# Kernel tuning notes

Measured on AMD Instinct MI355X. Metric: run time of the kernel, lower is better.

Reference implementation:

```python
import jax, jax.numpy as jnp
import numpy as np

N_C = 50000
N_N = 50000
E = 500000
D = 128


def _graph_conv(x_src, src, dst, n_src, n_dst, W, b):
    # DGL GraphConv, norm='both': symmetric degree normalization, then linear.
    ones = jnp.ones(src.shape, x_src.dtype)
    deg_out = jax.ops.segment_sum(ones, src, num_segments=n_src)
    deg_in = jax.ops.segment_sum(ones, dst, num_segments=n_dst)
    norm_src = jnp.maximum(deg_out, 1.0) ** -0.5  # [n_src]
    norm_dst = jnp.maximum(deg_in, 1.0) ** -0.5   # [n_dst]
    m = (x_src * norm_src[:, None])[src]          # [E, D] gather
    agg = jax.ops.segment_sum(m, dst, num_segments=n_dst)  # [n_dst, D]
    return (agg * norm_dst[:, None]) @ W + b


def _sage_conv(x_src, x_dst, src, dst, n_dst, W_self, W_neigh, b):
    # DGL SAGEConv, aggregator='mean': fc_self(h_dst) + fc_neigh(mean_neigh) + bias.
    ones = jnp.ones(src.shape, x_src.dtype)
    deg_in = jnp.maximum(jax.ops.segment_sum(ones, dst, num_segments=n_dst), 1.0)
    h_neigh = jax.ops.segment_sum(x_src[src], dst, num_segments=n_dst) / deg_in[:, None]
    return x_dst @ W_self + h_neigh @ W_neigh + b


def setup_inputs() -> dict:
    key = jax.random.key(0)
    ks = jax.random.split(key, 20)
    s = 1.0 / np.sqrt(D)
    inp = {
        'feat_C': jax.random.normal(ks[0], (N_C, D), jnp.float32),
        'feat_N': jax.random.normal(ks[1], (N_N, D), jnp.float32),
        'W1_cc': jax.random.normal(ks[2], (D, D), jnp.float32) * s,
        'b1_cc': jnp.zeros((D,), jnp.float32),
        'W1_cn': jax.random.normal(ks[3], (D, D), jnp.float32) * s,
        'b1_cn': jnp.zeros((D,), jnp.float32),
        'W1_self': jax.random.normal(ks[4], (D, D), jnp.float32) * s,
        'W1_neigh': jax.random.normal(ks[5], (D, D), jnp.float32) * s,
        'b1_nn': jnp.zeros((D,), jnp.float32),
        'W2_cc': jax.random.normal(ks[6], (D, D), jnp.float32) * s,
        'b2_cc': jnp.zeros((D,), jnp.float32),
        'W2_cn': jax.random.normal(ks[7], (D, D), jnp.float32) * s,
        'b2_cn': jnp.zeros((D,), jnp.float32),
        'W2_self': jax.random.normal(ks[8], (D, D), jnp.float32) * s,
        'W2_neigh': jax.random.normal(ks[9], (D, D), jnp.float32) * s,
        'b2_nn': jnp.zeros((D,), jnp.float32),
        'cc_src': jax.random.randint(ks[10], (E,), 0, N_C),
        'cc_dst': jax.random.randint(ks[11], (E,), 0, N_C),
        'cn_src': jax.random.randint(ks[12], (E,), 0, N_C),
        'cn_dst': jax.random.randint(ks[13], (E,), 0, N_N),
        'nn_src': jax.random.randint(ks[14], (E,), 0, N_N),
        'nn_dst': jax.random.randint(ks[15], (E,), 0, N_N),
    }
    return inp


def reference(feat_C, feat_N, W1_cc, b1_cc, W1_cn, b1_cn, W1_self, W1_neigh, b1_nn,
              W2_cc, b2_cc, W2_cn, b2_cn, W2_self, W2_neigh, b2_nn,
              cc_src, cc_dst, cn_src, cn_dst, nn_src, nn_dst):
    # layer 1 (HeteroGraphConv, aggregate='sum') + relu
    hC = _graph_conv(feat_C, cc_src, cc_dst, N_C, N_C, W1_cc, b1_cc)
    hN = (_graph_conv(feat_C, cn_src, cn_dst, N_C, N_N, W1_cn, b1_cn)
          + _sage_conv(feat_N, feat_N, nn_src, nn_dst, N_N, W1_self, W1_neigh, b1_nn))
    hC = jax.nn.relu(hC)
    hN = jax.nn.relu(hN)
    # layer 2
    oC = _graph_conv(hC, cc_src, cc_dst, N_C, N_C, W2_cc, b2_cc)
    oN = (_graph_conv(hC, cn_src, cn_dst, N_C, N_N, W2_cn, b2_cn)
          + _sage_conv(hN, hN, nn_src, nn_dst, N_N, W2_self, W2_neigh, b2_nn))
    return oC, oN
```

## Files before the change

kernel.cpp:

```cpp
#include <hip/hip_runtime.h>

#define NCN 50000
#define NE  500000
#define DF  128

#define BSHIFT 9
#define NBUCK 98
#define BK 128
#define CAP 7168
#define CHUNK 4096

typedef __attribute__((ext_vector_type(8))) short mfrag;
typedef __attribute__((ext_vector_type(4))) float facc4;

__device__ inline ushort f2bf(float x) {
    unsigned u = __float_as_uint(x);
    unsigned r = (u + 0x7FFFu + ((u >> 16) & 1u)) >> 16;
    return (ushort)r;
}
__device__ inline float bf2f(ushort h) { return __uint_as_float(((unsigned)h) << 16); }

__device__ inline void store_split(ushort* __restrict__ T, int row, int lane,
                                   float vx, float vy) {
    ushort hx = f2bf(vx); ushort lx = f2bf(vx - bf2f(hx));
    ushort hy = f2bf(vy); ushort ly = f2bf(vy - bf2f(hy));
    uint hp = (uint)hx | ((uint)hy << 16);
    uint lp = (uint)lx | ((uint)ly << 16);
    *(uint*)(T + (size_t)row * DF + lane * 2) = hp;
    *(uint*)(T + (size_t)NCN * DF + (size_t)row * DF + lane * 2) = lp;
}

__global__ __launch_bounds__(256) void hist2_k(
    const int* __restrict__ cc_src, const int* __restrict__ cn_src,
    int* __restrict__ cnt2)
{
    int i = blockIdx.x * 256 + threadIdx.x;
    if (i >= NE) return;
    atomicAdd(&cnt2[cc_src[i]], 1);
    atomicAdd(&cnt2[NCN + cn_src[i]], 1);
}

__global__ __launch_bounds__(256) void srcnorm_k(
    const int* __restrict__ cnt2, float* __restrict__ snorm2, int n2)
{
    int i = blockIdx.x * 256 + threadIdx.x;
    if (i >= n2) return;
    int c = cnt2[i]; if (c < 1) c = 1;
    snorm2[i] = rsqrtf((float)c);
}

__global__ __launch_bounds__(256) void binA_k(
    const int* __restrict__ cc_src, const int* __restrict__ cc_dst,
    const int* __restrict__ cn_src, const int* __restrict__ cn_dst,
    const int* __restrict__ nn_src, const int* __restrict__ nn_dst,
    uint2* __restrict__ R, int* __restrict__ bc)
{
    const int s = blockIdx.y;
    const int* key; const int* pay;
    switch (s) {
      case 0: key = cc_dst; pay = cc_src; break;
      case 1: key = cn_dst; pay = cn_src; break;
      default: key = nn_dst; pay = nn_src; break;
    }
    __shared__ uint2 rec[CHUNK];
    __shared__ int lhist[BK], lofs[BK], lcur[BK], gbase[BK];
    __shared__ int ls[256];
    const int tid = threadIdx.x;
    const int base = blockIdx.x * CHUNK;

    int k[16], p[16];
    #pragma unroll
    for (int j = 0; j < 16; ++j) {
        int e = base + j * 256 + tid;
        bool valid = (e < NE);
        k[j] = valid ? key[e] : -1;
        p[j] = valid ? pay[e] : 0;
    }
    if (tid < BK) lhist[tid] = 0;
    __syncthreads();
    #pragma unroll
    for (int j = 0; j < 16; ++j)
        if (k[j] >= 0) atomicAdd(&lhist[k[j] >> BSHIFT], 1);
    __syncthreads();
    int v = (tid < BK) ? lhist[tid] : 0;
    ls[tid] = v;
    __syncthreads();
    #pragma unroll
    for (int off = 1; off < 128; off <<= 1) {
        int t = (tid >= off) ? ls[tid - off] : 0;
        __syncthreads();
        ls[tid] += t;
        __syncthreads();
    }
    if (tid < BK) { int e = ls[tid] - v; lofs[tid] = e; lcur[tid] = e; }
    __syncthreads();
    #pragma unroll
    for (int j = 0; j < 16; ++j) {
        if (k[j] >= 0) {
            int b = k[j] >> BSHIFT;
            int pos = atomicAdd(&lcur[b], 1);
            rec[pos] = make_uint2((unsigned)k[j], (unsigned)p[j]);
        }
    }
    __syncthreads();
    if (tid < BK) {
        int c = lcur[tid] - lofs[tid];
        gbase[tid] = (c > 0) ? atomicAdd(&bc[s * BK + tid], c) : 0;
    }
    __syncthreads();
    int total = ls[127];
    for (int i = tid; i < total; i += 256) {
        uint2 r = rec[i];
        int b = (int)(r.x >> BSHIFT);
        int gi = gbase[b] + (i - lofs[b]);
        R[((size_t)s * NBUCK + b) * CAP + gi] = r;
    }
}

__global__ __launch_bounds__(256) void binB_k(
    const uint2* __restrict__ R, const int* __restrict__ bc,
    int* __restrict__ rp3, int* __restrict__ col3)
{
    const int b = blockIdx.x;
    const int s = blockIdx.y;
    const int tid = threadIdx.x;
    __shared__ int cnt[512];
    __shared__ int lofs[512];
    __shared__ int ls[256];
    __shared__ int sbase;

    const int nrec = bc[s * BK + b];
    const uint2* rec = R + ((size_t)s * NBUCK + b) * CAP;

    for (int i = tid; i < 512; i += 256) cnt[i] = 0;
    __syncthreads();
    for (int i = tid; i < nrec; i += 256)
        atomicAdd(&cnt[rec[i].x & 511], 1);
    __syncthreads();

    {
        int v = (tid < b) ? bc[s * BK + tid] : 0;
        ls[tid] = v;
        __syncthreads();
        for (int off = 128; off > 0; off >>= 1) {
            if (tid < off) ls[tid] += ls[tid + off];
            __syncthreads();
        }
        if (tid == 0) sbase = ls[0];
        __syncthreads();
    }
    const int colBase = sbase;

    int v0 = cnt[2 * tid], v1 = cnt[2 * tid + 1];
    int pairSum = v0 + v1;
    ls[tid] = pairSum;
    __syncthreads();
    #pragma unroll
    for (int off = 1; off < 256; off <<= 1) {
        int t = (tid >= off) ? ls[tid - off] : 0;
        __syncthreads();
        ls[tid] += t;
        __syncthreads();
    }
    int excl = ls[tid] - pairSum;
    lofs[2 * tid] = excl;
    lofs[2 * tid + 1] = excl + v0;
    __syncthreads();
    const int total = ls[255];

    int* rp = rp3 + (size_t)s * (NCN + 1);
    for (int j = tid; j < 512; j += 256) {
        int d = b * 512 + j;
        if (d < NCN) rp[d] = colBase + lofs[j];
    }
    if (b == NBUCK - 1 && tid == 0) rp[NCN] = colBase + total;
    __syncthreads();

    int* col = col3 + (size_t)s * NE + colBase;
    for (int i = tid; i < nrec; i += 256) {
        uint2 r = rec[i];
        int pos = atomicAdd(&lofs[r.x & 511], 1);
        col[pos] = (int)r.y;
    }
}

__global__ __launch_bounds__(256) void wconv_k(
    const float* __restrict__ Wm0, const float* __restrict__ Wm1,
    const float* __restrict__ Wm2, const float* __restrict__ Wm3,
    const float* __restrict__ Wm4, const float* __restrict__ Wm5,
    const float* __restrict__ Wm6, const float* __restrict__ Wm7,
    ushort* __restrict__ out)
{
    const float* Ws[8] = {Wm0, Wm1, Wm2, Wm3, Wm4, Wm5, Wm6, Wm7};
    const float* W = Ws[blockIdx.x];
    ushort* o = out + (size_t)blockIdx.x * 32768;
    for (int i = threadIdx.x; i < 16384; i += 256) {
        int c = i >> 13;
        int r = i & 8191;
        int n = r >> 6;
        int jj = r & 63;
        int kk = c * 64 + (jj ^ ((n & 7) << 3));
        float wv = W[kk * 128 + n];
        ushort h = f2bf(wv);
        float lv = wv - bf2f(h);
        o[c * 16384 + r] = h;
        o[c * 16384 + 8192 + r] = f2bf(lv);
    }
}

__global__ __launch_bounds__(256) void agg_k(
    const float* __restrict__ X0, const int* __restrict__ rp0,
    const int* __restrict__ col0, const float* __restrict__ sc0,
    ushort* __restrict__ out0,
    const float* __restrict__ X1, const int* __restrict__ rp1,
    const int* __restrict__ col1, const float* __restrict__ sc1,
    ushort* __restrict__ out1,
    const float* __restrict__ X2, const int* __restrict__ rp2,
    const int* __restrict__ col2, const float* __restrict__ sc2,
    ushort* __restrict__ out2)
{
    const float* X; const int* rp; const int* col; const float* sc; ushort* out;
    if (blockIdx.y == 0)      { X = X0; rp = rp0; col = col0; sc = sc0; out = out0; }
    else if (blockIdx.y == 1) { X = X1; rp = rp1; col = col1; sc = sc1; out = out1; }
    else                      { X = X2; rp = rp2; col = col2; sc = sc2; out = out2; }

    int gid = blockIdx.x * 256 + threadIdx.x;
    int row = gid >> 6;
    int lane = threadIdx.x & 63;
    if (row >= NCN) return;
    int e0 = rp[row], e1 = rp[row + 1];
    float ax = 0.f, ay = 0.f;
    int e = e0;
    for (; e + 4 <= e1; e += 4) {
        int s0 = col[e], s1 = col[e + 1], s2 = col[e + 2], s3 = col[e + 3];
        float c0 = sc ? sc[s0] : 1.0f;
        float c1 = sc ? sc[s1] : 1.0f;
        float c2 = sc ? sc[s2] : 1.0f;
        float c3 = sc ? sc[s3] : 1.0f;
        const float2 u0 = *(const float2*)(X + (size_t)s0 * DF + lane * 2);
        const float2 u1 = *(const float2*)(X + (size_t)s1 * DF + lane * 2);
        const float2 u2 = *(const float2*)(X + (size_t)s2 * DF + lane * 2);
        const float2 u3 = *(const float2*)(X + (size_t)s3 * DF + lane * 2);
        ax = fmaf(u0.x, c0, ax); ay = fmaf(u0.y, c0, ay);
        ax = fmaf(u1.x, c1, ax); ay = fmaf(u1.y, c1, ay);
        ax = fmaf(u2.x, c2, ax); ay = fmaf(u2.y, c2, ay);
        ax = fmaf(u3.x, c3, ax); ay = fmaf(u3.y, c3, ay);
    }
    for (; e < e1; ++e) {
        int s0 = col[e];
        float c0 = sc ? sc[s0] : 1.0f;
        const float2 u0 = *(const float2*)(X + (size_t)s0 * DF + lane * 2);
        ax = fmaf(u0.x, c0, ax); ay = fmaf(u0.y, c0, ay);
    }
    int deg = e1 - e0; if (deg < 1) deg = 1;
    float dsc = sc ? rsqrtf((float)deg) : (1.0f / (float)deg);
    store_split(out, row, lane, ax * dsc, ay * dsc);
}

template<int NSRC, bool RELU, int F32S>
__global__ __launch_bounds__(256, 4) void mgemm_k(
    const void* __restrict__ A0, const void* __restrict__ A1, const void* __restrict__ A2,
    const ushort* __restrict__ Wi0, const ushort* __restrict__ Wi1, const ushort* __restrict__ Wi2,
    const float* __restrict__ b0, const float* __restrict__ b1,
    float* __restrict__ Y, int M)
{
    constexpr int NCH = 2 * NSRC;
    __shared__ ushort Wsm[16384];
    const int tid = threadIdx.x;
    const int l = tid & 63;
    const int wv = tid >> 6;
    const int r0 = blockIdx.x * 128;

    const void*   Aarr[3] = {A0, A1, A2};
    const ushort* Warr[3] = {Wi0, Wi1, Wi2};

    int arow[2];
    #pragma unroll
    for (int rt = 0; rt < 2; ++rt) {
        int r = r0 + wv * 32 + rt * 16 + (l & 15);
        arow[rt] = (r < M) ? r : (M - 1);
    }
    const int kgrp = (l >> 4) * 8;

    facc4 acc[2][8];
    #pragma unroll
    for (int rt = 0; rt < 2; ++rt)
        #pragma unroll
        for (int ct = 0; ct < 8; ++ct)
            acc[rt][ct] = (facc4){0.f, 0.f, 0.f, 0.f};

    uint4 Wr[8];
    auto loadWr = [&](int c) {
        int s = c >> 1, half = c & 1;
        const uint4* wp = (const uint4*)(Warr[s] + half * 16384);
        #pragma unroll
        for (int i = 0; i < 8; ++i) Wr[i] = wp[i * 256 + tid];
    };

    mfrag ah[2][2], al[2][2];
    auto loadA = [&](int c) {
        int s = c >> 1;
        int k0 = (c & 1) * 64;
        if (s == F32S) {
            const float* F = (const float*)Aarr[s];
            #pragma unroll
            for (int ks = 0; ks < 2; ++ks)
                #pragma unroll
                for (int rt = 0; rt < 2; ++rt) {
                    const float* p = F + (size_t)arow[rt] * DF + k0 + ks * 32 + kgrp;
                    float4 v0 = *(const float4*)p;
                    float4 v1 = *(const float4*)(p + 4);
                    union { mfrag m; ushort u[8]; } H, L;
                    float vv0[4] = {v0.x, v0.y, v0.z, v0.w};
                    float vv1[4] = {v1.x, v1.y, v1.z, v1.w};
                    #pragma unroll
                    for (int j = 0; j < 4; ++j) {
                        ushort h = f2bf(vv0[j]);
                        H.u[j] = h; L.u[j] = f2bf(vv0[j] - bf2f(h));
                    }
                    #pragma unroll
                    for (int j = 0; j < 4; ++j) {
                        ushort h = f2bf(vv1[j]);
                        H.u[4 + j] = h; L.u[4 + j] = f2bf(vv1[j] - bf2f(h));
                    }
                    ah[ks][rt] = H.m; al[ks][rt] = L.m;
                }
        } else {
            const ushort* T = (const ushort*)Aarr[s];
            #pragma unroll
            for (int ks = 0; ks < 2; ++ks)
                #pragma unroll
                for (int rt = 0; rt < 2; ++rt) {
                    size_t o = (size_t)arow[rt] * DF + k0 + ks * 32 + kgrp;
                    ah[ks][rt] = *(const mfrag*)(T + o);
                    al[ks][rt] = *(const mfrag*)(T + (size_t)NCN * DF + o);
                }
        }
    };

    loadWr(0);
    #pragma unroll
    for (int c = 0; c < NCH; ++c) {
        __syncthreads();
        {
            uint4* wd = (uint4*)Wsm;
            #pragma unroll
            for (int i = 0; i < 8; ++i) wd[i * 256 + tid] = Wr[i];
        }
        loadA(c);
        if (c + 1 < NCH) loadWr(c + 1);
        __syncthreads();
        #pragma unroll
        for (int ks = 0; ks < 2; ++ks) {
            const int kbyte = ks * 64 + (l >> 4) * 16;
            #pragma unroll
            for (int ct = 0; ct < 8; ++ct) {
                int colc = ct * 16 + (l & 15);
                int widx = colc * 64 + ((kbyte ^ ((colc & 7) << 4)) >> 1);
                mfrag w_hi = *(const mfrag*)(Wsm + widx);
                mfrag w_lo = *(const mfrag*)(Wsm + 8192 + widx);
                #pragma unroll
                for (int rt = 0; rt < 2; ++rt) {
                    acc[rt][ct] = __builtin_amdgcn_mfma_f32_16x16x32_bf16(ah[ks][rt], w_hi, acc[rt][ct], 0, 0, 0);
                    acc[rt][ct] = __builtin_amdgcn_mfma_f32_16x16x32_bf16(ah[ks][rt], w_lo, acc[rt][ct], 0, 0, 0);
                    acc[rt][ct] = __builtin_amdgcn_mfma_f32_16x16x32_bf16(al[ks][rt], w_hi, acc[rt][ct], 0, 0, 0);
                }
            }
        }
    }
    __syncthreads();

    float bias[8];
    #pragma unroll
    for (int ct = 0; ct < 8; ++ct) {
        int colc = ct * 16 + (l & 15);
        float bv = b0 ? b0[colc] : 0.f;
        if (b1) bv += b1[colc];
        bias[ct] = bv;
    }
    #pragma unroll
    for (int rt = 0; rt < 2; ++rt) {
        #pragma unroll
        for (int q = 0; q < 4; ++q) {
            int row = r0 + wv * 32 + rt * 16 + (l >> 4) * 4 + q;
            if (row < M) {
                #pragma unroll
                for (int ct = 0; ct < 8; ++ct) {
                    float v = acc[rt][ct][q] + bias[ct];
                    if (RELU) v = fmaxf(v, 0.f);
                    Y[(size_t)row * DF + ct * 16 + (l & 15)] = v;
                }
            }
        }
    }
}

extern "C" void kernel_launch(void* const* d_in, const int* in_sizes, int n_in,
                              void* d_out, int out_size, void* d_ws, size_t ws_size,
                              hipStream_t stream)
{
    (void)in_sizes; (void)n_in; (void)out_size; (void)ws_size;
    const float* feat_C   = (const float*)d_in[0];
    const float* feat_N   = (const float*)d_in[1];
    const float* W1_cc    = (const float*)d_in[2];
    const float* b1_cc    = (const float*)d_in[3];
    const float* W1_cn    = (const float*)d_in[4];
    const float* b1_cn    = (const float*)d_in[5];
    const float* W1_self  = (const float*)d_in[6];
    const float* W1_neigh = (const float*)d_in[7];
    const float* b1_nn    = (const float*)d_in[8];
    const float* W2_cc    = (const float*)d_in[9];
    const float* b2_cc    = (const float*)d_in[10];
    const float* W2_cn    = (const float*)d_in[11];
    const float* b2_cn    = (const float*)d_in[12];
    const float* W2_self  = (const float*)d_in[13];
    const float* W2_neigh = (const float*)d_in[14];
    const float* b2_nn    = (const float*)d_in[15];
    const int* cc_src = (const int*)d_in[16];
    const int* cc_dst = (const int*)d_in[17];
    const int* cn_src = (const int*)d_in[18];
    const int* cn_dst = (const int*)d_in[19];
    const int* nn_src = (const int*)d_in[20];
    const int* nn_dst = (const int*)d_in[21];

    char* ws = (char*)d_ws;
    size_t off = 0;
    auto take = [&](size_t bytes) -> char* {
        char* p = ws + off;
        off = (off + bytes + 255) & ~(size_t)255;
        return p;
    };
    int*    rp3    = (int*)take((size_t)3 * (NCN + 1) * sizeof(int));
    int*    col3   = (int*)take((size_t)3 * NE * sizeof(int));
    float*  snorm2 = (float*)take((size_t)2 * NCN * sizeof(float));
    int*    cnt2   = (int*)take((size_t)2 * NCN * sizeof(int));
    int*    bc     = (int*)take((size_t)3 * BK * sizeof(int));
    ushort* Wimg   = (ushort*)take((size_t)8 * 32768 * sizeof(ushort));
    char* bigRegion = take((size_t)2 * 2 * NCN * DF * sizeof(ushort));
    uint2*  R  = (uint2*)bigRegion;
    ushort* P0 = (ushort*)bigRegion;
    ushort* P1 = (ushort*)(bigRegion + (size_t)2 * NCN * DF * sizeof(ushort));

    float* oC = (float*)d_out;
    float* oN = oC + (size_t)NCN * DF;
    ushort* oCsplit = (ushort*)oC;

    const int edgeBlocks = (NE + 255) / 256;
    const int binABlocks = (NE + CHUNK - 1) / CHUNK;
    const int aggBlocks  = (NCN * 64 + 255) / 256;
    const int gemmBlocks = (NCN + 127) / 128;

    auto img = [&](int m) { return (const ushort*)(Wimg + (size_t)m * 32768); };
    const int* rpCC = rp3 + 0 * (NCN + 1);
    const int* rpCN = rp3 + 1 * (NCN + 1);
    const int* rpNN = rp3 + 2 * (NCN + 1);
    const int* colCC = col3 + 0 * NE;
    const int* colCN = col3 + 1 * NE;
    const int* colNN = col3 + 2 * NE;
    const float* snCC = snorm2 + 0 * NCN;
    const float* snCN = snorm2 + 1 * NCN;

    hipMemsetAsync(cnt2, 0, (size_t)2 * NCN * sizeof(int), stream);
    hipMemsetAsync(bc, 0, (size_t)3 * BK * sizeof(int), stream);
    hist2_k<<<edgeBlocks, 256, 0, stream>>>(cc_src, cn_src, cnt2);
    srcnorm_k<<<(2 * NCN + 255) / 256, 256, 0, stream>>>(cnt2, snorm2, 2 * NCN);
    binA_k<<<dim3(binABlocks, 3), 256, 0, stream>>>(cc_src, cc_dst, cn_src, cn_dst,
                                                    nn_src, nn_dst, R, bc);
    binB_k<<<dim3(NBUCK, 3), 256, 0, stream>>>(R, bc, rp3, col3);
    wconv_k<<<8, 256, 0, stream>>>(W1_cc, W1_cn, W1_neigh, W1_self,
                                   W2_cc, W2_cn, W2_neigh, W2_self, Wimg);

    agg_k<<<dim3(aggBlocks, 3), 256, 0, stream>>>(
        feat_C, rpCC, colCC, snCC, P0,
        feat_C, rpCN, colCN, snCN, P1,
        feat_N, rpNN, colNN, nullptr, oCsplit);
    mgemm_k<3, true, 2><<<gemmBlocks, 256, 0, stream>>>(P1, oCsplit, feat_N,
                                                        img(1), img(2), img(3),
                                                        b1_cn, b1_nn, oN, NCN);
    mgemm_k<1, true, -1><<<gemmBlocks, 256, 0, stream>>>(P0, nullptr, nullptr,
                                                         img(0), nullptr, nullptr,
                                                         b1_cc, nullptr, oC, NCN);

    agg_k<<<dim3(aggBlocks, 2), 256, 0, stream>>>(
        oC, rpCC, colCC, snCC, P0,
        oC, rpCN, colCN, snCN, P1,
        nullptr, nullptr, nullptr, nullptr, nullptr);
    agg_k<<<dim3(aggBlocks, 1), 256, 0, stream>>>(
        oN, rpNN, colNN, nullptr, oCsplit,
        nullptr, nullptr, nullptr, nullptr, nullptr,
        nullptr, nullptr, nullptr, nullptr, nullptr);
    mgemm_k<3, false, 2><<<gemmBlocks, 256, 0, stream>>>(P1, oCsplit, oN,
                                                         img(5), img(6), img(7),
                                                         b2_cn, b2_nn, oN, NCN);
    mgemm_k<1, false, -1><<<gemmBlocks, 256, 0, stream>>>(P0, nullptr, nullptr,
                                                          img(4), nullptr, nullptr,
                                                          b2_cc, nullptr, oC, NCN);
}
```

Baseline: 485.2 us.

## Aggregate two rows per wave with float4 gathers and double-buffer GEMM A loads

The aggregation kernel now gives each half-wave one destination row and gathers 16-byte float4 chunks per lane. Neighbour indices and scales are loaded cooperatively once per 32-edge chunk and broadcast with shuffles, which cuts redundant index and scale loads and widens memory transactions. The GEMM kernel double-buffers the A fragments so the next chunk's A load overlaps the current MFMA work. Its occupancy hint drops from 4 to 3 blocks to make room for the extra registers, trading occupancy for overlap.

```diff
diff --git a/kernel.cpp b/kernel.cpp
--- a/kernel.cpp
+++ b/kernel.cpp
@@ -20,14 +20,16 @@
 }
 __device__ inline float bf2f(ushort h) { return __uint_as_float(((unsigned)h) << 16); }
 
-__device__ inline void store_split(ushort* __restrict__ T, int row, int lane,
-                                   float vx, float vy) {
-    ushort hx = f2bf(vx); ushort lx = f2bf(vx - bf2f(hx));
-    ushort hy = f2bf(vy); ushort ly = f2bf(vy - bf2f(hy));
-    uint hp = (uint)hx | ((uint)hy << 16);
-    uint lp = (uint)lx | ((uint)ly << 16);
-    *(uint*)(T + (size_t)row * DF + lane * 2) = hp;
-    *(uint*)(T + (size_t)NCN * DF + (size_t)row * DF + lane * 2) = lp;
+__device__ inline void store_split4(ushort* __restrict__ T, int row, int lane4,
+                                    float4 v) {
+    ushort h0 = f2bf(v.x); ushort l0 = f2bf(v.x - bf2f(h0));
+    ushort h1 = f2bf(v.y); ushort l1 = f2bf(v.y - bf2f(h1));
+    ushort h2 = f2bf(v.z); ushort l2 = f2bf(v.z - bf2f(h2));
+    ushort h3 = f2bf(v.w); ushort l3 = f2bf(v.w - bf2f(h3));
+    uint2 hp = make_uint2((uint)h0 | ((uint)h1 << 16), (uint)h2 | ((uint)h3 << 16));
+    uint2 lp = make_uint2((uint)l0 | ((uint)l1 << 16), (uint)l2 | ((uint)l3 << 16));
+    *(uint2*)(T + (size_t)row * DF + lane4 * 4) = hp;
+    *(uint2*)(T + (size_t)NCN * DF + (size_t)row * DF + lane4 * 4) = lp;
 }
 
 __global__ __launch_bounds__(256) void hist2_k(
@@ -224,41 +226,55 @@
     else if (blockIdx.y == 1) { X = X1; rp = rp1; col = col1; sc = sc1; out = out1; }
     else                      { X = X2; rp = rp2; col = col2; sc = sc2; out = out2; }
 
-    int gid = blockIdx.x * 256 + threadIdx.x;
-    int row = gid >> 6;
-    int lane = threadIdx.x & 63;
+    int wid = (blockIdx.x * 256 + threadIdx.x) >> 6;
+    int half = (threadIdx.x >> 5) & 1;
+    int lane4 = threadIdx.x & 31;
+    int row = wid * 2 + half;
     if (row >= NCN) return;
     int e0 = rp[row], e1 = rp[row + 1];
-    float ax = 0.f, ay = 0.f;
+    const bool useSc = (sc != nullptr);
+    float4 a = make_float4(0.f, 0.f, 0.f, 0.f);
     int e = e0;
-    for (; e + 4 <= e1; e += 4) {
-        int s0 = col[e], s1 = col[e + 1], s2 = col[e + 2], s3 = col[e + 3];
-        float c0 = sc ? sc[s0] : 1.0f;
-        float c1 = sc ? sc[s1] : 1.0f;
-        float c2 = sc ? sc[s2] : 1.0f;
-        float c3 = sc ? sc[s3] : 1.0f;
-        const float2 u0 = *(const float2*)(X + (size_t)s0 * DF + lane * 2);
-        const float2 u1 = *(const float2*)(X + (size_t)s1 * DF + lane * 2);
-        const float2 u2 = *(const float2*)(X + (size_t)s2 * DF + lane * 2);
-        const float2 u3 = *(const float2*)(X + (size_t)s3 * DF + lane * 2);
-        ax = fmaf(u0.x, c0, ax); ay = fmaf(u0.y, c0, ay);
-        ax = fmaf(u1.x, c1, ax); ay = fmaf(u1.y, c1, ay);
-        ax = fmaf(u2.x, c2, ax); ay = fmaf(u2.y, c2, ay);
-        ax = fmaf(u3.x, c3, ax); ay = fmaf(u3.y, c3, ay);
-    }
-    for (; e < e1; ++e) {
-        int s0 = col[e];
-        float c0 = sc ? sc[s0] : 1.0f;
-        const float2 u0 = *(const float2*)(X + (size_t)s0 * DF + lane * 2);
-        ax = fmaf(u0.x, c0, ax); ay = fmaf(u0.y, c0, ay);
+    while (e < e1) {
+        int cnt = e1 - e; if (cnt > 32) cnt = 32;
+        int myc = (lane4 < cnt) ? col[e + lane4] : 0;
+        float mysc = (useSc && lane4 < cnt) ? sc[myc] : 1.0f;
+        int j = 0;
+        for (; j + 4 <= cnt; j += 4) {
+            int s0 = __shfl(myc, j, 32),     s1 = __shfl(myc, j + 1, 32);
+            int s2 = __shfl(myc, j + 2, 32), s3 = __shfl(myc, j + 3, 32);
+            float c0 = __shfl(mysc, j, 32),     c1 = __shfl(mysc, j + 1, 32);
+            float c2 = __shfl(mysc, j + 2, 32), c3 = __shfl(mysc, j + 3, 32);
+            const float4 u0 = *(const float4*)(X + (size_t)s0 * DF + lane4 * 4);
+            const float4 u1 = *(const float4*)(X + (size_t)s1 * DF + lane4 * 4);
+            const float4 u2 = *(const float4*)(X + (size_t)s2 * DF + lane4 * 4);
+            const float4 u3 = *(const float4*)(X + (size_t)s3 * DF + lane4 * 4);
+            a.x = fmaf(u0.x, c0, a.x); a.y = fmaf(u0.y, c0, a.y);
+            a.z = fmaf(u0.z, c0, a.z); a.w = fmaf(u0.w, c0, a.w);
+            a.x = fmaf(u1.x, c1, a.x); a.y = fmaf(u1.y, c1, a.y);
+            a.z = fmaf(u1.z, c1, a.z); a.w = fmaf(u1.w, c1, a.w);
+            a.x = fmaf(u2.x, c2, a.x); a.y = fmaf(u2.y, c2, a.y);
+            a.z = fmaf(u2.z, c2, a.z); a.w = fmaf(u2.w, c2, a.w);
+            a.x = fmaf(u3.x, c3, a.x); a.y = fmaf(u3.y, c3, a.y);
+            a.z = fmaf(u3.z, c3, a.z); a.w = fmaf(u3.w, c3, a.w);
+        }
+        for (; j < cnt; ++j) {
+            int s0 = __shfl(myc, j, 32);
+            float c0 = __shfl(mysc, j, 32);
+            const float4 u0 = *(const float4*)(X + (size_t)s0 * DF + lane4 * 4);
+            a.x = fmaf(u0.x, c0, a.x); a.y = fmaf(u0.y, c0, a.y);
+            a.z = fmaf(u0.z, c0, a.z); a.w = fmaf(u0.w, c0, a.w);
+        }
+        e += cnt;
     }
     int deg = e1 - e0; if (deg < 1) deg = 1;
-    float dsc = sc ? rsqrtf((float)deg) : (1.0f / (float)deg);
-    store_split(out, row, lane, ax * dsc, ay * dsc);
+    float dsc = useSc ? rsqrtf((float)deg) : (1.0f / (float)deg);
+    a.x *= dsc; a.y *= dsc; a.z *= dsc; a.w *= dsc;
+    store_split4(out, row, lane4, a);
 }
 
 template<int NSRC, bool RELU, int F32S>
-__global__ __launch_bounds__(256, 4) void mgemm_k(
+__global__ __launch_bounds__(256, 3) void mgemm_k(
     const void* __restrict__ A0, const void* __restrict__ A1, const void* __restrict__ A2,
     const ushort* __restrict__ Wi0, const ushort* __restrict__ Wi1, const ushort* __restrict__ Wi2,
     const float* __restrict__ b0, const float* __restrict__ b1,
@@ -291,14 +307,14 @@
 
     uint4 Wr[8];
     auto loadWr = [&](int c) {
-        int s = c >> 1, half = c & 1;
-        const uint4* wp = (const uint4*)(Warr[s] + half * 16384);
+        int s = c >> 1, chalf = c & 1;
+        const uint4* wp = (const uint4*)(Warr[s] + chalf * 16384);
         #pragma unroll
         for (int i = 0; i < 8; ++i) Wr[i] = wp[i * 256 + tid];
     };
 
-    mfrag ah[2][2], al[2][2];
-    auto loadA = [&](int c) {
+    mfrag ahA[2][2], alA[2][2], ahB[2][2], alB[2][2];
+    auto loadA = [&](int c, mfrag (&ah)[2][2], mfrag (&al)[2][2]) {
         int s = c >> 1;
         int k0 = (c & 1) * 64;
         if (s == F32S) {
@@ -338,18 +354,7 @@
         }
     };
 
-    loadWr(0);
-    #pragma unroll
-    for (int c = 0; c < NCH; ++c) {
-        __syncthreads();
-        {
-            uint4* wd = (uint4*)Wsm;
-            #pragma unroll
-            for (int i = 0; i < 8; ++i) wd[i * 256 + tid] = Wr[i];
-        }
-        loadA(c);
-        if (c + 1 < NCH) loadWr(c + 1);
-        __syncthreads();
+    auto compute = [&](const mfrag (&ah)[2][2], const mfrag (&al)[2][2]) {
         #pragma unroll
         for (int ks = 0; ks < 2; ++ks) {
             const int kbyte = ks * 64 + (l >> 4) * 16;
@@ -367,6 +372,26 @@
                 }
             }
         }
+    };
+
+    loadWr(0);
+    loadA(0, ahA, alA);
+    #pragma unroll
+    for (int c = 0; c < NCH; ++c) {
+        __syncthreads();
+        {
+            uint4* wd = (uint4*)Wsm;
+            #pragma unroll
+            for (int i = 0; i < 8; ++i) wd[i * 256 + tid] = Wr[i];
+        }
+        if (c + 1 < NCH) {
+            loadWr(c + 1);
+            if ((c & 1) == 0) loadA(c + 1, ahB, alB);
+            else              loadA(c + 1, ahA, alA);
+        }
+        __syncthreads();
+        if ((c & 1) == 0) compute(ahA, alA);
+        else              compute(ahB, alB);
     }
     __syncthreads();
 
@@ -447,7 +472,7 @@
 
     const int edgeBlocks = (NE + 255) / 256;
     const int binABlocks = (NE + CHUNK - 1) / CHUNK;
-    const int aggBlocks  = (NCN * 64 + 255) / 256;
+    const int aggBlocks  = (((NCN + 1) / 2) * 64 + 255) / 256;
     const int gemmBlocks = (NCN + 127) / 128;
 
     auto img = [&](int m) { return (const ushort*)(Wimg + (size_t)m * 32768); };
```

After: 465.6 us. 1.04x faster.
